# Kernel tuning notes

Hardware: AMD Instinct MI355X
Metric: run time of the kernel (lower is better)

Reference implementation:

```python
import jax, jax.numpy as jnp
import numpy as np

DIM = 1024
HEADS = 16
DIM_HEAD = 64
DEPTH = 12
LN_EPS = 1e-5


def setup_inputs() -> dict:
    key = jax.random.key(0)
    k1, k2, k3 = jax.random.split(key, 3)
    B, N = 4, 2048
    inner = HEADS * DIM_HEAD
    x = jax.random.normal(k1, (B, N, DIM), dtype=jnp.float32)
    ln_w = jnp.ones((DIM,), jnp.float32)
    ln_b = jnp.zeros((DIM,), jnp.float32)
    w_qkv = jax.random.normal(k2, (DIM, 3 * inner), jnp.float32) * (DIM ** -0.5)
    w_out = jax.random.normal(k3, (inner, DIM), jnp.float32) * (inner ** -0.5)
    b_out = jnp.zeros((DIM,), jnp.float32)
    return {"x": x, "ln_w": ln_w, "ln_b": ln_b, "w_qkv": w_qkv,
            "w_out": w_out, "b_out": b_out, "layer_index": 2}


def reference(x, ln_w, ln_b, w_qkv, w_out, b_out, layer_index):
    B, N, D = x.shape
    scale = DIM_HEAD ** -0.5
    # LayerNorm
    mu = jnp.mean(x, axis=-1, keepdims=True)
    var = jnp.mean(jnp.square(x - mu), axis=-1, keepdims=True)
    xn = (x - mu) * jax.lax.rsqrt(var + LN_EPS) * ln_w + ln_b
    # QKV projection (no bias), split heads: b n (h d) -> b h n d
    qkv = xn @ w_qkv  # [B, N, 3*H*Dh]
    q, k, v = jnp.split(qkv, 3, axis=-1)
    def heads(t):
        return t.reshape(B, N, HEADS, DIM_HEAD).transpose(0, 2, 1, 3)
    q, k, v = heads(q), heads(k), heads(v)
    dots = jnp.einsum('bhnd,bhmd->bhnm', q, k) * scale  # [B,H,N,N]
    if layer_index < DEPTH // 2:
        attn = jax.nn.relu(dots)
    else:
        attn = jax.nn.softmax(dots, axis=-1)
    attn = attn / N  # divide by x.shape[1]
    out = jnp.einsum('bhnm,bhmd->bhnd', attn, v)
    out = out.transpose(0, 2, 1, 3).reshape(B, N, HEADS * DIM_HEAD)
    # to_out (heads > 1): Linear + (inactive) dropout
    return out @ w_out + b_out
```

## Files before the change

### kernel.cpp

```cpp
#include <hip/hip_runtime.h>
#include <stdint.h>

typedef __bf16 bf16x8 __attribute__((ext_vector_type(8)));
typedef __bf16 bf16x4 __attribute__((ext_vector_type(4)));
typedef float f32x4 __attribute__((ext_vector_type(4)));
typedef float f32x16 __attribute__((ext_vector_type(16)));

#define PSCALE (0.125f / 2048.0f)

#define GLOAD16(src, dst)                                                      \
  __builtin_amdgcn_global_load_lds(                                            \
      (__attribute__((address_space(1))) void*)const_cast<__bf16*>(src),       \
      (__attribute__((address_space(3))) void*)(dst), 16, 0, 0)

__global__ __launch_bounds__(256) void prep(
    const float* __restrict__ x, const float* __restrict__ lw,
    const float* __restrict__ lb, __bf16* __restrict__ xn,
    const float* __restrict__ w_qkv, __bf16* __restrict__ Wt1,
    const float* __restrict__ w_out, __bf16* __restrict__ Wt2) {
  __shared__ __bf16 T[64][72];
  __shared__ float red[8];
  const int b = blockIdx.x;
  const int t = threadIdx.x;
  if (b < 8192) {
    const float4 v = ((const float4*)(x + (size_t)b * 1024))[t];
    float s = v.x + v.y + v.z + v.w;
    float ss = v.x * v.x + v.y * v.y + v.z * v.z + v.w * v.w;
#pragma unroll
    for (int o = 32; o; o >>= 1) {
      s += __shfl_down(s, o);
      ss += __shfl_down(ss, o);
    }
    if ((t & 63) == 0) {
      red[t >> 6] = s;
      red[4 + (t >> 6)] = ss;
    }
    __syncthreads();
    const float tot = red[0] + red[1] + red[2] + red[3];
    const float tot2 = red[4] + red[5] + red[6] + red[7];
    const float mu = tot * (1.0f / 1024.0f);
    const float var = tot2 * (1.0f / 1024.0f) - mu * mu;
    const float rs = rsqrtf(var + 1e-5f);
    const float4 wv = ((const float4*)lw)[t];
    const float4 bv = ((const float4*)lb)[t];
    bf16x4 o;
    o[0] = (__bf16)((v.x - mu) * rs * wv.x + bv.x);
    o[1] = (__bf16)((v.y - mu) * rs * wv.y + bv.y);
    o[2] = (__bf16)((v.z - mu) * rs * wv.z + bv.z);
    o[3] = (__bf16)((v.w - mu) * rs * wv.w + bv.w);
    ((bf16x4*)xn)[(size_t)b * 256 + t] = o;
    return;
  }
  const float* A;
  __bf16* At;
  int R, C, bx, by;
  if (b < 8960) {
    const int ti = b - 8192;
    A = w_qkv; At = Wt1; R = 1024; C = 3072;
    bx = ti % 48; by = ti / 48;
  } else {
    const int ti = b - 8960;
    A = w_out; At = Wt2; R = 1024; C = 1024;
    bx = ti % 16; by = ti / 16;
  }
  const int rb = by * 64, cb = bx * 64;
  const int r = t >> 2, cg = t & 3;
#pragma unroll
  for (int k = 0; k < 4; ++k) {
    const float4 v =
        *(const float4*)(A + (size_t)(rb + r) * C + cb + cg * 16 + k * 4);
    T[cg * 16 + k * 4 + 0][r] = (__bf16)v.x;
    T[cg * 16 + k * 4 + 1][r] = (__bf16)v.y;
    T[cg * 16 + k * 4 + 2][r] = (__bf16)v.z;
    T[cg * 16 + k * 4 + 3][r] = (__bf16)v.w;
  }
  __syncthreads();
#pragma unroll
  for (int i = 0; i < 2; ++i) {
    const int j = i * 256 + t;
    const int c = j >> 3, s8 = j & 7;
    const bf16x8 o = *(const bf16x8*)&T[c][s8 * 8];
    *(bf16x8*)(At + (size_t)(cb + c) * R + rb + s8 * 8) = o;
  }
}

template <int MODE>
__global__ __launch_bounds__(512) void gemm_nt(
    const __bf16* __restrict__ A, const __bf16* __restrict__ B, int K,
    float* __restrict__ outF, __bf16* __restrict__ Qo, __bf16* __restrict__ Ko,
    __bf16* __restrict__ Vto, const float* __restrict__ bias) {
  __shared__ __bf16 Sm[3 * 24576];
  const int tid = threadIdx.x;
  const int lane = tid & 63, w = tid >> 6;
  const int g = lane >> 4, c15 = lane & 15;
  const int wr = w >> 2, wc = w & 3;
  const int linear = blockIdx.y * gridDim.x + blockIdx.x;
  const int per = (gridDim.x * gridDim.y) >> 3;
  const int nl = (linear & 7) * per + (linear >> 3);
  const int rb = (nl / gridDim.x) * 128, cb = (nl % gridDim.x) * 256;

  const __bf16* aSp[2];
  const __bf16* bSp[4];
  int aDo[2], bDo[4];
#pragma unroll
  for (int i = 0; i < 2; ++i) {
    const int j = i * 512 + tid, row = j >> 3, slot = j & 7;
    aSp[i] = A + (size_t)(rb + row) * K + ((slot ^ (row & 7)) << 3);
    aDo[i] = i * 4096 + w * 512;
  }
#pragma unroll
  for (int i = 0; i < 4; ++i) {
    const int j = i * 512 + tid, col = j >> 3, slot = j & 7;
    bSp[i] = B + (size_t)(cb + col) * K + ((slot ^ (col & 7)) << 3);
    bDo[i] = 8192 + i * 4096 + w * 512;
  }

  f32x4 acc[4][4] = {};
  const int nkb = K >> 6;

#pragma unroll
  for (int t = 0; t < 2; ++t) {
    __bf16* dst = Sm + t * 24576;
#pragma unroll
    for (int i = 0; i < 2; ++i) GLOAD16(aSp[i] + t * 64, dst + aDo[i]);
#pragma unroll
    for (int i = 0; i < 4; ++i) GLOAD16(bSp[i] + t * 64, dst + bDo[i]);
  }

  int cur = 0, stg = 2, koff = 128;
  for (int kb = 0; kb < nkb; ++kb) {
    if (kb == nkb - 1) {
      asm volatile("s_waitcnt vmcnt(0)" ::: "memory");
    } else {
      asm volatile("s_waitcnt vmcnt(6)" ::: "memory");
    }
    __builtin_amdgcn_s_barrier();
    const bool do_stage = (kb < nkb - 2);
    __bf16* sdst = Sm + stg * 24576;
    if (do_stage) {
#pragma unroll
      for (int i = 0; i < 2; ++i) GLOAD16(aSp[i] + koff, sdst + aDo[i]);
    }
    const __bf16* __restrict__ Ac = Sm + cur * 24576;
    const __bf16* __restrict__ Bc = Ac + 8192;
    {
      bf16x8 af[4], bfr[4];
      const int kc = g;
#pragma unroll
      for (int rt = 0; rt < 4; ++rt) {
        const int lr = wr * 64 + rt * 16 + c15;
        af[rt] = *(const bf16x8*)(Ac + lr * 64 + ((kc ^ (lr & 7)) << 3));
      }
#pragma unroll
      for (int ct = 0; ct < 4; ++ct) {
        const int lc = wc * 64 + ct * 16 + c15;
        bfr[ct] = *(const bf16x8*)(Bc + lc * 64 + ((kc ^ (lc & 7)) << 3));
      }
      __builtin_amdgcn_s_setprio(1);
#pragma unroll
      for (int rt = 0; rt < 4; ++rt)
#pragma unroll
        for (int ct = 0; ct < 4; ++ct)
          acc[rt][ct] = __builtin_amdgcn_mfma_f32_16x16x32_bf16(
              af[rt], bfr[ct], acc[rt][ct], 0, 0, 0);
      __builtin_amdgcn_s_setprio(0);
    }
    if (do_stage) {
#pragma unroll
      for (int i = 0; i < 4; ++i) GLOAD16(bSp[i] + koff, sdst + bDo[i]);
      koff += 64;
    }
    {
      bf16x8 af[4], bfr[4];
      const int kc = 4 + g;
#pragma unroll
      for (int rt = 0; rt < 4; ++rt) {
        const int lr = wr * 64 + rt * 16 + c15;
        af[rt] = *(const bf16x8*)(Ac + lr * 64 + ((kc ^ (lr & 7)) << 3));
      }
#pragma unroll
      for (int ct = 0; ct < 4; ++ct) {
        const int lc = wc * 64 + ct * 16 + c15;
        bfr[ct] = *(const bf16x8*)(Bc + lc * 64 + ((kc ^ (lc & 7)) << 3));
      }
      __builtin_amdgcn_s_setprio(1);
#pragma unroll
      for (int rt = 0; rt < 4; ++rt)
#pragma unroll
        for (int ct = 0; ct < 4; ++ct)
          acc[rt][ct] = __builtin_amdgcn_mfma_f32_16x16x32_bf16(
              af[rt], bfr[ct], acc[rt][ct], 0, 0, 0);
      __builtin_amdgcn_s_setprio(0);
    }
    cur = (cur == 2) ? 0 : cur + 1;
    stg = (stg == 2) ? 0 : stg + 1;
  }
  const int r00 = rb + wr * 64 + g * 4;
  if (MODE == 1) {
#pragma unroll
    for (int ct = 0; ct < 4; ++ct) {
      const int col = cb + wc * 64 + ct * 16 + c15;
      const float bv = bias[col];
#pragma unroll
      for (int rt = 0; rt < 4; ++rt) {
        const int row = r00 + rt * 16;
#pragma unroll
        for (int r = 0; r < 4; ++r)
          outF[(size_t)(row + r) * 1024 + col] = acc[rt][ct][r] + bv;
      }
    }
  } else {
#pragma unroll
    for (int ct = 0; ct < 4; ++ct) {
      const int col = cb + wc * 64 + ct * 16 + c15;
      const int part = col >> 10, rem = col & 1023;
      const int h = rem >> 6, d = rem & 63;
#pragma unroll
      for (int rt = 0; rt < 4; ++rt) {
        const int row = r00 + rt * 16;
        const int bi = row >> 11, n = row & 2047;
        const size_t bh = (size_t)bi * 16 + h;
        if (part == 2) {
          bf16x4 pv;
#pragma unroll
          for (int r = 0; r < 4; ++r) pv[r] = (__bf16)acc[rt][ct][r];
          *(bf16x4*)(Vto + (bh * 64 + d) * 2048 + n) = pv;
        } else if (part == 0) {
          __bf16* dst = Qo + (bh * 2048 + n) * 64 + d;
#pragma unroll
          for (int r = 0; r < 4; ++r)
            dst[(size_t)r * 64] = (__bf16)(acc[rt][ct][r] * PSCALE);
        } else {
          __bf16* dst = Ko + (bh * 2048 + n) * 64 + d;
#pragma unroll
          for (int r = 0; r < 4; ++r) dst[(size_t)r * 64] = (__bf16)acc[rt][ct][r];
        }
      }
    }
  }
}

__global__ __launch_bounds__(512, 4) void attn_relu(
    const __bf16* __restrict__ Q, const __bf16* __restrict__ K,
    const __bf16* __restrict__ Vt, __bf16* __restrict__ O) {
  __shared__ __bf16 Ks[2][128 * 64];
  __shared__ __bf16 Vs[2][64 * 128];
  const int tid = threadIdx.x;
  const int lane = tid & 63, wv = tid >> 6;
  const int hi = lane >> 5, c31 = lane & 31;
  const int bh = blockIdx.x, qb = blockIdx.y;
  const __bf16* Qg = Q + ((size_t)bh * 2048 + qb * 256) * 64;
  const __bf16* Kg = K + (size_t)bh * 2048 * 64;
  const __bf16* Vg = Vt + (size_t)bh * 64 * 2048;

  const __bf16* kp0;
  const __bf16* kp1;
  const __bf16* vp0;
  const __bf16* vp1;
  {
    const int j0 = tid, j1 = 512 + tid;
    const int X0 = j0 >> 3, s0 = j0 & 7;
    const int X1 = j1 >> 3, s1 = j1 & 7;
    const int K0 = (X0 & ~12) | ((X0 & 4) << 1) | ((X0 & 8) >> 1);
    const int K1 = (X1 & ~12) | ((X1 & 4) << 1) | ((X1 & 8) >> 1);
    kp0 = Kg + (size_t)K0 * 64 + ((s0 ^ (X0 & 7) ^ ((X0 >> 3) & 3)) << 3);
    kp1 = Kg + (size_t)K1 * 64 + ((s1 ^ (X1 & 7) ^ ((X1 >> 3) & 3)) << 3);
    const int d0_ = j0 >> 4, t0_ = j0 & 15;
    const int d1_ = j1 >> 4, t1_ = j1 & 15;
    vp0 = Vg + (size_t)d0_ * 2048 + ((t0_ ^ (d0_ & 15) ^ ((d0_ >> 3) & 3)) << 3);
    vp1 = Vg + (size_t)d1_ * 2048 + ((t1_ ^ (d1_ & 15) ^ ((d1_ >> 3) & 3)) << 3);
  }
  const int dstoff = wv * 64 * 8;

  bf16x8 qf[4];
#pragma unroll
  for (int dw = 0; dw < 4; ++dw)
    qf[dw] = *(const bf16x8*)(Qg + (wv * 32 + c31) * 64 + dw * 16 + hi * 8);
  f32x16 oacc[2] = {};

  GLOAD16(kp0, Ks[0] + dstoff);
  GLOAD16(kp1, Ks[0] + 512 * 8 + dstoff);
  GLOAD16(vp0, Vs[0] + dstoff);
  GLOAD16(vp1, Vs[0] + 512 * 8 + dstoff);
  kp0 += 128 * 64; kp1 += 128 * 64; vp0 += 128; vp1 += 128;

  for (int kb = 0; kb < 16; ++kb) {
    const int cur = kb & 1;
    if (kb < 15) {
      GLOAD16(kp0, Ks[cur ^ 1] + dstoff);
      GLOAD16(kp1, Ks[cur ^ 1] + 512 * 8 + dstoff);
      GLOAD16(vp0, Vs[cur ^ 1] + dstoff);
      GLOAD16(vp1, Vs[cur ^ 1] + 512 * 8 + dstoff);
      kp0 += 128 * 64; kp1 += 128 * 64; vp0 += 128; vp1 += 128;
      asm volatile("s_waitcnt vmcnt(4)" ::: "memory");
    } else {
      asm volatile("s_waitcnt vmcnt(0)" ::: "memory");
    }
    __builtin_amdgcn_s_barrier();
    const __bf16* __restrict__ Kc = Ks[cur];
    const __bf16* __restrict__ Vc = Vs[cur];
#pragma unroll
    for (int kb32 = 0; kb32 < 4; ++kb32) {
      bf16x8 kf[4];
      const int R = kb32 * 32 + c31;
#pragma unroll
      for (int dw = 0; dw < 4; ++dw)
        kf[dw] = *(const bf16x8*)(
            Kc + R * 64 + (((2 * dw + hi) ^ (R & 7) ^ ((R >> 3) & 3)) << 3));
      f32x16 s = {};
      __builtin_amdgcn_s_setprio(1);
#pragma unroll
      for (int dw = 0; dw < 4; ++dw)
        s = __builtin_amdgcn_mfma_f32_32x32x16_bf16(kf[dw], qf[dw], s, 0, 0, 0);
      __builtin_amdgcn_s_setprio(0);
      bf16x8 pa[2];
#pragma unroll
      for (int wl = 0; wl < 2; ++wl)
#pragma unroll
        for (int e = 0; e < 8; ++e)
          pa[wl][e] = (__bf16)fmaxf(s[8 * wl + e], 0.0f);
      __builtin_amdgcn_s_setprio(1);
#pragma unroll
      for (int wl = 0; wl < 2; ++wl) {
        const int win = 2 * kb32 + wl;
#pragma unroll
        for (int dc = 0; dc < 2; ++dc) {
          const int d = dc * 32 + c31;
          const bf16x8 vb = *(const bf16x8*)(
              Vc + d * 128 +
              (((2 * win + hi) ^ (d & 15) ^ ((d >> 3) & 3)) << 3));
          oacc[dc] = __builtin_amdgcn_mfma_f32_32x32x16_bf16(pa[wl], vb,
                                                             oacc[dc], 0, 0, 0);
        }
      }
      __builtin_amdgcn_s_setprio(0);
    }
    __builtin_amdgcn_s_barrier();
  }
  const int bi = bh >> 4, h = bh & 15;
#pragma unroll
  for (int dc = 0; dc < 2; ++dc) {
    const int col = h * 64 + dc * 32 + c31;
#pragma unroll
    for (int r = 0; r < 16; ++r) {
      const int q = wv * 32 + (r & 3) + 8 * (r >> 2) + 4 * hi;
      const int n0 = qb * 256 + q;
      O[((size_t)bi * 2048 + n0) * 1024 + col] = (__bf16)oacc[dc][r];
    }
  }
}

extern "C" void kernel_launch(void* const* d_in, const int* in_sizes, int n_in,
                              void* d_out, int out_size, void* d_ws,
                              size_t ws_size, hipStream_t stream) {
  (void)in_sizes; (void)n_in; (void)out_size; (void)ws_size;
  const float* x = (const float*)d_in[0];
  const float* ln_w = (const float*)d_in[1];
  const float* ln_b = (const float*)d_in[2];
  const float* w_qkv = (const float*)d_in[3];
  const float* w_out = (const float*)d_in[4];
  const float* b_out = (const float*)d_in[5];
  char* ws = (char*)d_ws;
  __bf16* xn = (__bf16*)(ws);
  __bf16* Wt1 = (__bf16*)(ws + (size_t)(16u << 20));
  __bf16* Wt2 = (__bf16*)(ws + (size_t)(22u << 20));
  __bf16* Qb = (__bf16*)(ws + (size_t)(24u << 20));
  __bf16* Kb = (__bf16*)(ws + (size_t)(40u << 20));
  __bf16* Vtb = (__bf16*)(ws + (size_t)(56u << 20));
  __bf16* Ob = (__bf16*)(ws + (size_t)(72u << 20));
  float* out = (float*)d_out;

  prep<<<9216, 256, 0, stream>>>(x, ln_w, ln_b, xn, w_qkv, Wt1, w_out, Wt2);
  gemm_nt<0><<<dim3(12, 64), 512, 0, stream>>>(xn, Wt1, 1024, nullptr, Qb, Kb,
                                               Vtb, nullptr);
  attn_relu<<<dim3(64, 8), 512, 0, stream>>>(Qb, Kb, Vtb, Ob);
  gemm_nt<1><<<dim3(4, 64), 512, 0, stream>>>(Ob, Wt2, 1024, out, nullptr,
                                              nullptr, nullptr, b_out);
}
```

Measured before the change: 161.4 us.

## Split attention key blocks across wave pairs with Q streamed from fragment layout

Q is now written by the projection kernel in an MFMA-fragment-friendly layout and read from global memory inside the loop instead of being held in registers. Each pair of waves covers 64 query rows and splits each 128-key block between its two waves, so every loaded K fragment is reused for two query tiles. The partial outputs are reduced through shared memory at the end. The next-block prefetch moves to mid-iteration with a full vmcnt(0) wait. The aim is to raise K/V fragment reuse and overlap loads with compute, at the cost of repeated Q global loads, more accumulator registers and an extra reduction pass.

After: 254.2 us. 1.57x slower.

```diff
diff --git a/kernel.cpp b/kernel.cpp
--- a/kernel.cpp
+++ b/kernel.cpp
@@ -226,10 +226,13 @@
           for (int r = 0; r < 4; ++r) pv[r] = (__bf16)acc[rt][ct][r];
           *(bf16x4*)(Vto + (bh * 64 + d) * 2048 + n) = pv;
         } else if (part == 0) {
-          __bf16* dst = Qo + (bh * 2048 + n) * 64 + d;
-#pragma unroll
-          for (int r = 0; r < 4; ++r)
-            dst[(size_t)r * 64] = (__bf16)(acc[rt][ct][r] * PSCALE);
+          const int dw2 = (((d >> 4) << 1) | ((d >> 3) & 1));
+#pragma unroll
+          for (int r = 0; r < 4; ++r) {
+            const int nn = n + r;
+            Qo[bh * 131072 + (size_t)(nn >> 5) * 2048 + dw2 * 256 +
+               (nn & 31) * 8 + (d & 7)] = (__bf16)(acc[rt][ct][r] * PSCALE);
+          }
         } else {
           __bf16* dst = Ko + (bh * 2048 + n) * 64 + d;
 #pragma unroll
@@ -241,17 +244,20 @@
 }
 
 __global__ __launch_bounds__(512, 4) void attn_relu(
-    const __bf16* __restrict__ Q, const __bf16* __restrict__ K,
+    const __bf16* __restrict__ Qf, const __bf16* __restrict__ K,
     const __bf16* __restrict__ Vt, __bf16* __restrict__ O) {
-  __shared__ __bf16 Ks[2][128 * 64];
-  __shared__ __bf16 Vs[2][64 * 128];
+  __shared__ __align__(16) float redF[16384];
+  __bf16* Sb = (__bf16*)redF;
   const int tid = threadIdx.x;
   const int lane = tid & 63, wv = tid >> 6;
   const int hi = lane >> 5, c31 = lane & 31;
+  const int pair = wv >> 1, half = wv & 1;
   const int bh = blockIdx.x, qb = blockIdx.y;
-  const __bf16* Qg = Q + ((size_t)bh * 2048 + qb * 256) * 64;
   const __bf16* Kg = K + (size_t)bh * 2048 * 64;
   const __bf16* Vg = Vt + (size_t)bh * 64 * 2048;
+  const __bf16* Q0 = Qf + (size_t)bh * 131072 +
+                     (size_t)(qb * 8 + pair * 2) * 2048 + hi * 256 + c31 * 8;
+  const __bf16* Q1 = Q0 + 2048;
 
   const __bf16* kp0;
   const __bf16* kp1;
@@ -270,39 +276,27 @@
     vp0 = Vg + (size_t)d0_ * 2048 + ((t0_ ^ (d0_ & 15) ^ ((d0_ >> 3) & 3)) << 3);
     vp1 = Vg + (size_t)d1_ * 2048 + ((t1_ ^ (d1_ & 15) ^ ((d1_ >> 3) & 3)) << 3);
   }
-  const int dstoff = wv * 64 * 8;
-
-  bf16x8 qf[4];
-#pragma unroll
-  for (int dw = 0; dw < 4; ++dw)
-    qf[dw] = *(const bf16x8*)(Qg + (wv * 32 + c31) * 64 + dw * 16 + hi * 8);
-  f32x16 oacc[2] = {};
-
-  GLOAD16(kp0, Ks[0] + dstoff);
-  GLOAD16(kp1, Ks[0] + 512 * 8 + dstoff);
-  GLOAD16(vp0, Vs[0] + dstoff);
-  GLOAD16(vp1, Vs[0] + 512 * 8 + dstoff);
+  const int dstoff = wv * 512;
+
+  f32x16 oacc[2][2] = {};
+
+  GLOAD16(kp0, Sb + dstoff);
+  GLOAD16(kp1, Sb + 4096 + dstoff);
+  GLOAD16(vp0, Sb + 16384 + dstoff);
+  GLOAD16(vp1, Sb + 16384 + 4096 + dstoff);
   kp0 += 128 * 64; kp1 += 128 * 64; vp0 += 128; vp1 += 128;
 
   for (int kb = 0; kb < 16; ++kb) {
     const int cur = kb & 1;
-    if (kb < 15) {
-      GLOAD16(kp0, Ks[cur ^ 1] + dstoff);
-      GLOAD16(kp1, Ks[cur ^ 1] + 512 * 8 + dstoff);
-      GLOAD16(vp0, Vs[cur ^ 1] + dstoff);
-      GLOAD16(vp1, Vs[cur ^ 1] + 512 * 8 + dstoff);
-      kp0 += 128 * 64; kp1 += 128 * 64; vp0 += 128; vp1 += 128;
-      asm volatile("s_waitcnt vmcnt(4)" ::: "memory");
-    } else {
-      asm volatile("s_waitcnt vmcnt(0)" ::: "memory");
-    }
+    asm volatile("s_waitcnt vmcnt(0)" ::: "memory");
     __builtin_amdgcn_s_barrier();
-    const __bf16* __restrict__ Kc = Ks[cur];
-    const __bf16* __restrict__ Vc = Vs[cur];
-#pragma unroll
-    for (int kb32 = 0; kb32 < 4; ++kb32) {
+    const __bf16* __restrict__ Kc = Sb + cur * 8192;
+    const __bf16* __restrict__ Vc = Sb + 16384 + cur * 8192;
+#pragma unroll
+    for (int sub = 0; sub < 2; ++sub) {
+      const int kb32 = 2 * half + sub;
+      const int R = kb32 * 32 + c31;
       bf16x8 kf[4];
-      const int R = kb32 * 32 + c31;
 #pragma unroll
       for (int dw = 0; dw < 4; ++dw)
         kf[dw] = *(const bf16x8*)(
@@ -310,15 +304,31 @@
       f32x16 s = {};
       __builtin_amdgcn_s_setprio(1);
 #pragma unroll
-      for (int dw = 0; dw < 4; ++dw)
-        s = __builtin_amdgcn_mfma_f32_32x32x16_bf16(kf[dw], qf[dw], s, 0, 0, 0);
+      for (int dw = 0; dw < 4; ++dw) {
+        const bf16x8 q = *(const bf16x8*)(Q0 + dw * 512);
+        s = __builtin_amdgcn_mfma_f32_32x32x16_bf16(kf[dw], q, s, 0, 0, 0);
+      }
       __builtin_amdgcn_s_setprio(0);
-      bf16x8 pa[2];
+      bf16x8 p0[2];
 #pragma unroll
       for (int wl = 0; wl < 2; ++wl)
 #pragma unroll
         for (int e = 0; e < 8; ++e)
-          pa[wl][e] = (__bf16)fmaxf(s[8 * wl + e], 0.0f);
+          p0[wl][e] = (__bf16)fmaxf(s[8 * wl + e], 0.0f);
+      f32x16 s2 = {};
+      __builtin_amdgcn_s_setprio(1);
+#pragma unroll
+      for (int dw = 0; dw < 4; ++dw) {
+        const bf16x8 q = *(const bf16x8*)(Q1 + dw * 512);
+        s2 = __builtin_amdgcn_mfma_f32_32x32x16_bf16(kf[dw], q, s2, 0, 0, 0);
+      }
+      __builtin_amdgcn_s_setprio(0);
+      bf16x8 p1[2];
+#pragma unroll
+      for (int wl = 0; wl < 2; ++wl)
+#pragma unroll
+        for (int e = 0; e < 8; ++e)
+          p1[wl][e] = (__bf16)fmaxf(s2[8 * wl + e], 0.0f);
       __builtin_amdgcn_s_setprio(1);
 #pragma unroll
       for (int wl = 0; wl < 2; ++wl) {
@@ -329,24 +339,65 @@
           const bf16x8 vb = *(const bf16x8*)(
               Vc + d * 128 +
               (((2 * win + hi) ^ (d & 15) ^ ((d >> 3) & 3)) << 3));
-          oacc[dc] = __builtin_amdgcn_mfma_f32_32x32x16_bf16(pa[wl], vb,
-                                                             oacc[dc], 0, 0, 0);
+          oacc[0][dc] = __builtin_amdgcn_mfma_f32_32x32x16_bf16(
+              p0[wl], vb, oacc[0][dc], 0, 0, 0);
+          oacc[1][dc] = __builtin_amdgcn_mfma_f32_32x32x16_bf16(
+              p1[wl], vb, oacc[1][dc], 0, 0, 0);
         }
       }
       __builtin_amdgcn_s_setprio(0);
+      if (sub == 0 && kb < 15) {
+        const int nxt = cur ^ 1;
+        GLOAD16(kp0, Sb + nxt * 8192 + dstoff);
+        GLOAD16(kp1, Sb + nxt * 8192 + 4096 + dstoff);
+        GLOAD16(vp0, Sb + 16384 + nxt * 8192 + dstoff);
+        GLOAD16(vp1, Sb + 16384 + nxt * 8192 + 4096 + dstoff);
+        kp0 += 128 * 64; kp1 += 128 * 64; vp0 += 128; vp1 += 128;
+      }
     }
     __builtin_amdgcn_s_barrier();
   }
-  const int bi = bh >> 4, h = bh & 15;
-#pragma unroll
-  for (int dc = 0; dc < 2; ++dc) {
-    const int col = h * 64 + dc * 32 + c31;
-#pragma unroll
-    for (int r = 0; r < 16; ++r) {
-      const int q = wv * 32 + (r & 3) + 8 * (r >> 2) + 4 * hi;
-      const int n0 = qb * 256 + q;
-      O[((size_t)bi * 2048 + n0) * 1024 + col] = (__bf16)oacc[dc][r];
-    }
+  if (half) {
+#pragma unroll
+    for (int qg = 0; qg < 2; ++qg)
+#pragma unroll
+      for (int dc = 0; dc < 2; ++dc)
+#pragma unroll
+        for (int r4 = 0; r4 < 4; ++r4) {
+          f32x4 t;
+#pragma unroll
+          for (int j = 0; j < 4; ++j) t[j] = oacc[qg][dc][r4 * 4 + j];
+          *(f32x4*)(redF + pair * 4096 + (qg * 2 + dc) * 1024 + r4 * 256 +
+                    lane * 4) = t;
+        }
+  }
+  __builtin_amdgcn_s_barrier();
+  if (!half) {
+#pragma unroll
+    for (int qg = 0; qg < 2; ++qg)
+#pragma unroll
+      for (int dc = 0; dc < 2; ++dc)
+#pragma unroll
+        for (int r4 = 0; r4 < 4; ++r4) {
+          const f32x4 t = *(const f32x4*)(redF + pair * 4096 +
+                                          (qg * 2 + dc) * 1024 + r4 * 256 +
+                                          lane * 4);
+#pragma unroll
+          for (int j = 0; j < 4; ++j) oacc[qg][dc][r4 * 4 + j] += t[j];
+        }
+    const int bi = bh >> 4, h = bh & 15;
+#pragma unroll
+    for (int qg = 0; qg < 2; ++qg)
+#pragma unroll
+      for (int dc = 0; dc < 2; ++dc) {
+        const int col = h * 64 + dc * 32 + c31;
+#pragma unroll
+        for (int r = 0; r < 16; ++r) {
+          const int q = pair * 64 + qg * 32 + (r & 3) + 8 * (r >> 2) + 4 * hi;
+          const int n0 = qb * 256 + q;
+          O[((size_t)bi * 2048 + n0) * 1024 + col] = (__bf16)oacc[qg][dc][r];
+        }
+      }
   }
 }
 
```
